# Kernel tuning notes

Hardware: AMD Instinct MI355X
Metric: run time of the kernel (lower is better)

## Reference

```python
import jax, jax.numpy as jnp
import numpy as np

GRID_SIZE = 8
SCALE_SPLINE = 0.1
BATCH, IN_F, OUT_F = 2048, 1024, 1024


def setup_inputs() -> dict:
    key = jax.random.key(0)
    k1, k2, k3 = jax.random.split(key, 3)
    x = jax.random.normal(k1, (BATCH, IN_F), dtype=jnp.float32)
    # kaiming-uniform-ish scale for base linear weight
    bound = 1.0 / np.sqrt(IN_F)
    base_weight = jax.random.uniform(k2, (OUT_F, IN_F), dtype=jnp.float32,
                                     minval=-bound, maxval=bound)
    spline_coeff = 0.1 * jax.random.normal(k3, (OUT_F, IN_F, GRID_SIZE), dtype=jnp.float32)
    # grid buffer: identical linspace(-1,1,G+1) for every (out,in); keep 1-D
    grid = jnp.linspace(-1.0, 1.0, GRID_SIZE + 1, dtype=jnp.float32)
    return {"x": x, "base_weight": base_weight, "spline_coeff": spline_coeff, "grid": grid}


def reference(x, base_weight, spline_coeff, grid):
    # x: (B, I); base_weight: (O, I); spline_coeff: (O, I, G); grid: (G+1,)
    G = spline_coeff.shape[-1]
    base_out = x @ base_weight.T                       # (B, O)

    xc = jnp.clip(x, -1.0, 1.0)                        # (B, I)
    # bucketize: number of grid knots <= xc, minus 1, clamped to valid bin
    mask = xc[..., None] >= grid                       # (B, I, G+1)
    left_idx = jnp.clip(mask.sum(axis=-1) - 1, 0, G - 1)  # (B, I) int

    left_grid = grid[left_idx]                         # (B, I)
    right_grid = grid[left_idx + 1]                    # (B, I)
    denom = right_grid - left_grid
    denom = jnp.where(denom == 0, jnp.ones_like(denom), denom)
    weight = (xc - left_grid) / denom                  # (B, I)

    # coeff gather + weighted sum over in_features, expressed as a dense
    # contraction against a weight-scaled one-hot of the bin index:
    # spline_out[b,o] = sum_i spline_coeff[o,i,idx[b,i]] * weight[b,i]
    onehot_w = jax.nn.one_hot(left_idx, G, dtype=x.dtype) * weight[..., None]  # (B, I, G)
    spline_out = jnp.einsum('big,oig->bo', onehot_w, spline_coeff)             # (B, O)

    return base_out + SCALE_SPLINE * spline_out
```

## Files before the change

kernel.cpp:

```cpp
#include <hip/hip_runtime.h>
#include <stdint.h>

#define BATCH 2048
#define INF 1024
#define OUTF 1024
#define GRID_G 8
#define KTOT 9216

#define BM 256
#define BN 256
#define BK 64
#define SK 8
#define KC (KTOT / SK)
#define NKT (KC / BK)
#define MTT (BATCH / BM)
#define NTT (OUTF / BN)
#define CSLAB ((size_t)BATCH * OUTF)

typedef __attribute__((ext_vector_type(8))) short short8_t;
typedef __attribute__((ext_vector_type(4))) float f32x4_t;
typedef __attribute__((ext_vector_type(8))) unsigned short u16x8_t;

__device__ __forceinline__ unsigned short f2bf(float f) {
  unsigned int u = __float_as_uint(f);
  u += 0x7FFFu + ((u >> 16) & 1u);
  return (unsigned short)(u >> 16);
}

__device__ __forceinline__ void async16(void* lds, const void* g) {
  __builtin_amdgcn_global_load_lds(
      (const __attribute__((address_space(1))) void*)g,
      (__attribute__((address_space(3))) void*)lds, 16, 0, 0);
}

__global__ __launch_bounds__(256) void build_w_kernel(
    const float* __restrict__ bw, const float* __restrict__ coeff,
    unsigned short* __restrict__ wc) {
  int id = blockIdx.x * 256 + threadIdx.x;
  int row = id / (KTOT / 8);
  int k8 = id - row * (KTOT / 8);
  int k = k8 * 8;
  const float* src = (k < INF) ? (bw + (size_t)row * INF + k)
                               : (coeff + (size_t)row * (INF * GRID_G) + (k - INF));
  const float4* s4 = (const float4*)src;
  float4 a = s4[0], b = s4[1];
  u16x8_t v;
  v[0] = f2bf(a.x); v[1] = f2bf(a.y); v[2] = f2bf(a.z); v[3] = f2bf(a.w);
  v[4] = f2bf(b.x); v[5] = f2bf(b.y); v[6] = f2bf(b.z); v[7] = f2bf(b.w);
  *(u16x8_t*)(wc + (size_t)id * 8) = v;
}

__global__ __launch_bounds__(256) void build_a_kernel(
    const float* __restrict__ x, const float* __restrict__ grid,
    unsigned short* __restrict__ ac) {
  __shared__ float sg[GRID_G + 1];
  if (threadIdx.x <= GRID_G) sg[threadIdx.x] = grid[threadIdx.x];
  __syncthreads();
  int id = blockIdx.x * 256 + threadIdx.x;
  int b = id >> 10;
  int i = id & 1023;
  float xv = x[id];
  ac[(size_t)b * KTOT + i] = f2bf(xv);
  float xc = fminf(fmaxf(xv, -1.0f), 1.0f);
  int cnt = 0;
#pragma unroll
  for (int j = 0; j <= GRID_G; ++j) cnt += (xc >= sg[j]) ? 1 : 0;
  int idx = cnt - 1;
  idx = idx < 0 ? 0 : (idx > GRID_G - 1 ? GRID_G - 1 : idx);
  float left = sg[idx], right = sg[idx + 1];
  float denom = right - left;
  denom = (denom == 0.0f) ? 1.0f : denom;
  float w = (xc - left) / denom;
  unsigned short val = f2bf(0.1f * w);
  u16x8_t v;
#pragma unroll
  for (int g = 0; g < GRID_G; ++g) v[g] = (g == idx) ? val : (unsigned short)0;
  *(u16x8_t*)(ac + (size_t)b * KTOT + INF + (size_t)i * 8) = v;
}

__global__ __launch_bounds__(512, 2) void gemm_kernel(
    const unsigned short* __restrict__ A, const unsigned short* __restrict__ W,
    unsigned short* __restrict__ P) {
  __shared__ unsigned short LA[2][2][256 * 32];
  __shared__ unsigned short LB[2][2][256 * 32];

  int bid = blockIdx.x;
  int sk = bid & 7;
  int t0 = bid >> 3;
  int mt = t0 >> 2;
  int nt = t0 & 3;

  int tid = threadIdx.x;
  int wave = tid >> 6;
  int lane = tid & 63;
  int wr = wave >> 2, wc = wave & 3;
  int lr = lane & 15, lk = lane >> 4;
  int rlo = lk * 128 + lr * 8;

  int srow = (tid >> 6) * 16 + (tid & 15);
  int scol = ((tid >> 4) & 3) * 8;
  const unsigned short* gA  = A + (size_t)(mt * BM + srow) * KTOT + sk * KC + scol;
  const unsigned short* gA2 = gA + (size_t)128 * KTOT;
  const unsigned short* gB  = W + (size_t)(nt * BN + srow) * KTOT + sk * KC + scol;
  const unsigned short* gB2 = gB + (size_t)128 * KTOT;

  f32x4_t acc[2][4][4];
#pragma unroll
  for (int ch = 0; ch < 2; ++ch)
#pragma unroll
    for (int mf = 0; mf < 4; ++mf)
#pragma unroll
      for (int nf = 0; nf < 4; ++nf) acc[ch][mf][nf] = f32x4_t{0.f, 0.f, 0.f, 0.f};

#define STAGE_A(nb, ks_, tt) { \
    unsigned short* d_ = &LA[nb][ks_][wave * 512]; \
    async16(d_, gA + (tt) * BK + (ks_) * 32); \
    async16(d_ + 4096, gA2 + (tt) * BK + (ks_) * 32); }
#define STAGE_B(nb, ks_, tt) { \
    unsigned short* d_ = &LB[nb][ks_][wave * 512]; \
    async16(d_, gB + (tt) * BK + (ks_) * 32); \
    async16(d_ + 4096, gB2 + (tt) * BK + (ks_) * 32); }
#define LOAD_BF(ks_) { _Pragma("unroll") for (int nf = 0; nf < 4; ++nf) \
    bfr[nf] = *(const short8_t*)&LB[c][ks_][(wc * 4 + nf) * 512 + rlo]; }
#define LOAD_AF(ks_, ch_) { _Pragma("unroll") for (int mf = 0; mf < 4; ++mf) \
    afr[mf] = *(const short8_t*)&LA[c][ks_][(wr * 8 + (ch_) * 4 + mf) * 512 + rlo]; }
#define DO_MFMA(ch_) { __builtin_amdgcn_s_setprio(1); \
    _Pragma("unroll") for (int mf = 0; mf < 4; ++mf) \
    _Pragma("unroll") for (int nf = 0; nf < 4; ++nf) \
      acc[ch_][mf][nf] = __builtin_amdgcn_mfma_f32_16x16x32_bf16( \
          afr[mf], bfr[nf], acc[ch_][mf][nf], 0, 0, 0); \
    __builtin_amdgcn_s_setprio(0); }
#define GATE(pf_) { if (pf_) asm volatile("s_waitcnt vmcnt(4)" ::: "memory"); \
    else asm volatile("s_waitcnt vmcnt(0)" ::: "memory"); \
    __builtin_amdgcn_s_barrier(); \
    asm volatile("" ::: "memory"); }

  STAGE_A(0, 0, 0) STAGE_B(0, 0, 0) STAGE_A(0, 1, 0) STAGE_B(0, 1, 0)

  for (int t = 0; t < NKT; ++t) {
    int c = t & 1, nb = c ^ 1;
    int tn = t + 1;
    bool pf = tn < NKT;
    short8_t afr[4], bfr[4];

    GATE(pf)
    LOAD_AF(0, 0) LOAD_BF(0)
    if (pf) STAGE_A(nb, 0, tn)
    DO_MFMA(0)
    LOAD_AF(0, 1)
    if (pf) STAGE_B(nb, 0, tn)
    DO_MFMA(1)

    GATE(pf)
    LOAD_AF(1, 0) LOAD_BF(1)
    if (pf) STAGE_A(nb, 1, tn)
    DO_MFMA(0)
    LOAD_AF(1, 1)
    if (pf) STAGE_B(nb, 1, tn)
    DO_MFMA(1)
  }

  unsigned short* slab = P + (size_t)sk * CSLAB;
#pragma unroll
  for (int ch = 0; ch < 2; ++ch)
#pragma unroll
    for (int mf = 0; mf < 4; ++mf)
#pragma unroll
      for (int nf = 0; nf < 4; ++nf) {
        int col = nt * BN + wc * 64 + nf * 16 + lr;
        int rowb = mt * BM + wr * 128 + ch * 64 + mf * 16 + lk * 4;
#pragma unroll
        for (int r = 0; r < 4; ++r)
          slab[(size_t)(rowb + r) * OUTF + col] = f2bf(acc[ch][mf][nf][r]);
      }
}

__global__ __launch_bounds__(256) void reduce_kernel(
    const unsigned short* __restrict__ P, float* __restrict__ out) {
  size_t base = ((size_t)blockIdx.x * 256 + threadIdx.x) * 8;
  float s[8];
#pragma unroll
  for (int j = 0; j < 8; ++j) s[j] = 0.0f;
#pragma unroll
  for (int k = 0; k < SK; ++k) {
    u16x8_t v = *(const u16x8_t*)(P + (size_t)k * CSLAB + base);
#pragma unroll
    for (int j = 0; j < 8; ++j)
      s[j] += __uint_as_float((unsigned int)v[j] << 16);
  }
  float4 lo = {s[0], s[1], s[2], s[3]};
  float4 hi = {s[4], s[5], s[6], s[7]};
  *(float4*)(out + base) = lo;
  *(float4*)(out + base + 4) = hi;
}

extern "C" void kernel_launch(void* const* d_in, const int* in_sizes, int n_in,
                              void* d_out, int out_size, void* d_ws, size_t ws_size,
                              hipStream_t stream) {
  const float* x = (const float*)d_in[0];
  const float* bw = (const float*)d_in[1];
  const float* coeff = (const float*)d_in[2];
  const float* grid = (const float*)d_in[3];
  float* out = (float*)d_out;

  unsigned short* Acat = (unsigned short*)d_ws;
  unsigned short* Wcat = Acat + (size_t)BATCH * KTOT;
  unsigned short* Part = Wcat + (size_t)OUTF * KTOT;

  build_w_kernel<<<OUTF * (KTOT / 8) / 256, 256, 0, stream>>>(bw, coeff, Wcat);
  build_a_kernel<<<BATCH * INF / 256, 256, 0, stream>>>(x, grid, Acat);
  gemm_kernel<<<SK * MTT * NTT, 512, 0, stream>>>(Acat, Wcat, Part);
  reduce_kernel<<<(int)(CSLAB / 8 / 256), 256, 0, stream>>>(Part, out);
}
```

Before: 76.62 us.

## Restructure GEMM main loop into barrier-fenced phases with split LDS buffers

Replaces the indexed double-buffered LDS arrays with eight separately named buffers and unrolls the K loop by two, so buffer selection is static. Each K-half is split into phases. Every phase issues its LDS fragment reads and the next async global-to-LDS stage, then waits on lgkmcnt behind a sched_barrier and runs the MFMA block between two workgroup barriers. The vmcnt waits are moved to the B-staging phases. The aim is to make LDS reads, global prefetch and MFMA issue interleave more predictably across waves. The cost is many more barriers per K tile, which adds synchronisation stalls.

```diff
diff --git a/kernel.cpp b/kernel.cpp
--- a/kernel.cpp
+++ b/kernel.cpp
@@ -81,8 +81,10 @@
 __global__ __launch_bounds__(512, 2) void gemm_kernel(
     const unsigned short* __restrict__ A, const unsigned short* __restrict__ W,
     unsigned short* __restrict__ P) {
-  __shared__ unsigned short LA[2][2][256 * 32];
-  __shared__ unsigned short LB[2][2][256 * 32];
+  __shared__ unsigned short A0K0[256 * 32], A0K1[256 * 32];
+  __shared__ unsigned short A1K0[256 * 32], A1K1[256 * 32];
+  __shared__ unsigned short B0K0[256 * 32], B0K1[256 * 32];
+  __shared__ unsigned short B1K0[256 * 32], B1K1[256 * 32];
 
   int bid = blockIdx.x;
   int sk = bid & 7;
@@ -112,52 +114,60 @@
 #pragma unroll
       for (int nf = 0; nf < 4; ++nf) acc[ch][mf][nf] = f32x4_t{0.f, 0.f, 0.f, 0.f};
 
-#define STAGE_A(nb, ks_, tt) { \
-    unsigned short* d_ = &LA[nb][ks_][wave * 512]; \
-    async16(d_, gA + (tt) * BK + (ks_) * 32); \
-    async16(d_ + 4096, gA2 + (tt) * BK + (ks_) * 32); }
-#define STAGE_B(nb, ks_, tt) { \
-    unsigned short* d_ = &LB[nb][ks_][wave * 512]; \
-    async16(d_, gB + (tt) * BK + (ks_) * 32); \
-    async16(d_ + 4096, gB2 + (tt) * BK + (ks_) * 32); }
-#define LOAD_BF(ks_) { _Pragma("unroll") for (int nf = 0; nf < 4; ++nf) \
-    bfr[nf] = *(const short8_t*)&LB[c][ks_][(wc * 4 + nf) * 512 + rlo]; }
-#define LOAD_AF(ks_, ch_) { _Pragma("unroll") for (int mf = 0; mf < 4; ++mf) \
-    afr[mf] = *(const short8_t*)&LA[c][ks_][(wr * 8 + (ch_) * 4 + mf) * 512 + rlo]; }
-#define DO_MFMA(ch_) { __builtin_amdgcn_s_setprio(1); \
+#define DSR_AF(ARR, CH) { _Pragma("unroll") for (int mf = 0; mf < 4; ++mf) \
+    af[mf] = *(const short8_t*)&ARR[(wr * 8 + (CH) * 4 + mf) * 512 + rlo]; }
+#define DSR_BF(ARR) { _Pragma("unroll") for (int nf = 0; nf < 4; ++nf) \
+    bf[nf] = *(const short8_t*)&ARR[(wc * 4 + nf) * 512 + rlo]; }
+#define STAGE(DARR, CO) { \
+    unsigned short* d_ = &DARR[wave * 512]; \
+    async16(d_, gA_sel + (CO)); \
+    async16(d_ + 4096, gA2_sel + (CO)); }
+#define STAGEA(DARR, CO) { unsigned short* d_ = &DARR[wave * 512]; \
+    async16(d_, gA + (CO)); async16(d_ + 4096, gA2 + (CO)); }
+#define STAGEB(DARR, CO) { unsigned short* d_ = &DARR[wave * 512]; \
+    async16(d_, gB + (CO)); async16(d_ + 4096, gB2 + (CO)); }
+#define BAR() __builtin_amdgcn_s_barrier();
+#define LGKM0() { asm volatile("s_waitcnt lgkmcnt(0)" ::: "memory"); \
+    __builtin_amdgcn_sched_barrier(0); }
+#define MFMA16(CH) { __builtin_amdgcn_s_setprio(1); \
     _Pragma("unroll") for (int mf = 0; mf < 4; ++mf) \
     _Pragma("unroll") for (int nf = 0; nf < 4; ++nf) \
-      acc[ch_][mf][nf] = __builtin_amdgcn_mfma_f32_16x16x32_bf16( \
-          afr[mf], bfr[nf], acc[ch_][mf][nf], 0, 0, 0); \
+      acc[CH][mf][nf] = __builtin_amdgcn_mfma_f32_16x16x32_bf16( \
+          af[mf], bf[nf], acc[CH][mf][nf], 0, 0, 0); \
     __builtin_amdgcn_s_setprio(0); }
-#define GATE(pf_) { if (pf_) asm volatile("s_waitcnt vmcnt(4)" ::: "memory"); \
-    else asm volatile("s_waitcnt vmcnt(0)" ::: "memory"); \
-    __builtin_amdgcn_s_barrier(); \
-    asm volatile("" ::: "memory"); }
-
-  STAGE_A(0, 0, 0) STAGE_B(0, 0, 0) STAGE_A(0, 1, 0) STAGE_B(0, 1, 0)
-
-  for (int t = 0; t < NKT; ++t) {
-    int c = t & 1, nb = c ^ 1;
-    int tn = t + 1;
-    bool pf = tn < NKT;
-    short8_t afr[4], bfr[4];
-
-    GATE(pf)
-    LOAD_AF(0, 0) LOAD_BF(0)
-    if (pf) STAGE_A(nb, 0, tn)
-    DO_MFMA(0)
-    LOAD_AF(0, 1)
-    if (pf) STAGE_B(nb, 0, tn)
-    DO_MFMA(1)
-
-    GATE(pf)
-    LOAD_AF(1, 0) LOAD_BF(1)
-    if (pf) STAGE_A(nb, 1, tn)
-    DO_MFMA(0)
-    LOAD_AF(1, 1)
-    if (pf) STAGE_B(nb, 1, tn)
-    DO_MFMA(1)
+#define VM(pf_) { if (pf_) asm volatile("s_waitcnt vmcnt(4)" ::: "memory"); \
+    else asm volatile("s_waitcnt vmcnt(0)" ::: "memory"); }
+
+#define TILE(CA0, CA1, CB0, CB1, NA0, NA1, NB0, NB1, tt, pf_) { \
+    short8_t af[4], bf[4]; \
+    int ko = ((tt) + 1) * BK; \
+     \
+    DSR_BF(CB0) DSR_AF(CA0, 0) \
+    if (pf_) STAGEA(NA0, ko) \
+    BAR() LGKM0() MFMA16(0) BAR() \
+     \
+    DSR_AF(CA0, 1) \
+    if (pf_) STAGEB(NB0, ko) \
+    VM(pf_) BAR() LGKM0() MFMA16(1) BAR() \
+     \
+    DSR_BF(CB1) DSR_AF(CA1, 0) \
+    if (pf_) STAGEA(NA1, ko + 32) \
+    BAR() LGKM0() MFMA16(0) BAR() \
+     \
+    DSR_AF(CA1, 1) \
+    if (pf_) STAGEB(NB1, ko + 32) \
+    VM(pf_) BAR() LGKM0() MFMA16(1) BAR() \
+}
+
+  STAGEA(A0K0, 0) STAGEB(B0K0, 0) STAGEA(A0K1, 32) STAGEB(B0K1, 32)
+  VM(1)
+  BAR()
+
+  for (int i = 0; i < NKT / 2; ++i) {
+    int te = 2 * i, to = 2 * i + 1;
+    bool pfo = (to + 1) < NKT;
+    TILE(A0K0, A0K1, B0K0, B0K1, A1K0, A1K1, B1K0, B1K1, te, true)
+    TILE(A1K0, A1K1, B1K0, B1K1, A0K0, A0K1, B0K0, B0K1, to, pfo)
   }
 
   unsigned short* slab = P + (size_t)sk * CSLAB;
```

Result: slower. 81.19 us (+6.0%).

## Expand spline one-hot A operand in registers instead of materializing it

Applied to the files above, without the earlier changes.

The 9216-wide concatenated A matrix (bf16 x plus an 8-wide one-hot spline block) is no longer written out. The prep kernel now emits bf16 x and a packed 32-bit (weight, bin index) word per element. The GEMM stages these packed words into LDS and expands them into one-hot MFMA fragments in registers. This removes most of the A-side global write and read traffic. The cost is ALU work per fragment and a hand-unrolled, more intricate pipeline with custom waitcnt schedules.

```diff
diff --git a/kernel.cpp b/kernel.cpp
--- a/kernel.cpp
+++ b/kernel.cpp
@@ -7,14 +7,9 @@
 #define GRID_G 8
 #define KTOT 9216
 
-#define BM 256
-#define BN 256
-#define BK 64
 #define SK 8
-#define KC (KTOT / SK)
-#define NKT (KC / BK)
-#define MTT (BATCH / BM)
-#define NTT (OUTF / BN)
+#define MTT 8
+#define NTT 4
 #define CSLAB ((size_t)BATCH * OUTF)
 
 typedef __attribute__((ext_vector_type(8))) short short8_t;
@@ -31,6 +26,19 @@
   __builtin_amdgcn_global_load_lds(
       (const __attribute__((address_space(1))) void*)g,
       (__attribute__((address_space(3))) void*)lds, 16, 0, 0);
+}
+
+__device__ __forceinline__ short8_t onehot_frag(unsigned int p) {
+  unsigned int wlo = p & 0xFFFFu;
+  unsigned int idx = p >> 16;
+  unsigned int sel = (idx & 1u) ? (wlo << 16) : wlo;
+  unsigned int jt = idx >> 1;
+  union { unsigned int u[4]; short8_t s; } r;
+  r.u[0] = (jt == 0u) ? sel : 0u;
+  r.u[1] = (jt == 1u) ? sel : 0u;
+  r.u[2] = (jt == 2u) ? sel : 0u;
+  r.u[3] = (jt == 3u) ? sel : 0u;
+  return r.s;
 }
 
 __global__ __launch_bounds__(256) void build_w_kernel(
@@ -50,17 +58,15 @@
   *(u16x8_t*)(wc + (size_t)id * 8) = v;
 }
 
-__global__ __launch_bounds__(256) void build_a_kernel(
+__global__ __launch_bounds__(256) void build_apack_kernel(
     const float* __restrict__ x, const float* __restrict__ grid,
-    unsigned short* __restrict__ ac) {
+    unsigned short* __restrict__ xbf, unsigned int* __restrict__ ap) {
   __shared__ float sg[GRID_G + 1];
   if (threadIdx.x <= GRID_G) sg[threadIdx.x] = grid[threadIdx.x];
   __syncthreads();
   int id = blockIdx.x * 256 + threadIdx.x;
-  int b = id >> 10;
-  int i = id & 1023;
   float xv = x[id];
-  ac[(size_t)b * KTOT + i] = f2bf(xv);
+  xbf[id] = f2bf(xv);
   float xc = fminf(fmaxf(xv, -1.0f), 1.0f);
   int cnt = 0;
 #pragma unroll
@@ -71,38 +77,39 @@
   float denom = right - left;
   denom = (denom == 0.0f) ? 1.0f : denom;
   float w = (xc - left) / denom;
-  unsigned short val = f2bf(0.1f * w);
-  u16x8_t v;
-#pragma unroll
-  for (int g = 0; g < GRID_G; ++g) v[g] = (g == idx) ? val : (unsigned short)0;
-  *(u16x8_t*)(ac + (size_t)b * KTOT + INF + (size_t)i * 8) = v;
-}
-
-__global__ __launch_bounds__(512, 2) void gemm_kernel(
-    const unsigned short* __restrict__ A, const unsigned short* __restrict__ W,
-    unsigned short* __restrict__ P) {
+  ap[id] = (unsigned int)f2bf(0.1f * w) | ((unsigned int)idx << 16);
+}
+
+__global__ __launch_bounds__(512, 2) void fused_gemm_kernel(
+    const unsigned short* __restrict__ Xb, const unsigned int* __restrict__ Ap,
+    const unsigned short* __restrict__ Wc, unsigned short* __restrict__ P) {
   __shared__ unsigned short LA[2][2][256 * 32];
   __shared__ unsigned short LB[2][2][256 * 32];
 
   int bid = blockIdx.x;
   int sk = bid & 7;
-  int t0 = bid >> 3;
-  int mt = t0 >> 2;
-  int nt = t0 & 3;
-
-  int tid = threadIdx.x;
-  int wave = tid >> 6;
-  int lane = tid & 63;
+  int t0i = bid >> 3;
+  int mt = t0i >> 2, nt = t0i & 3;
+
+  int tid = threadIdx.x, wave = tid >> 6, lane = tid & 63;
   int wr = wave >> 2, wc = wave & 3;
   int lr = lane & 15, lk = lane >> 4;
   int rlo = lk * 128 + lr * 8;
 
-  int srow = (tid >> 6) * 16 + (tid & 15);
-  int scol = ((tid >> 4) & 3) * 8;
-  const unsigned short* gA  = A + (size_t)(mt * BM + srow) * KTOT + sk * KC + scol;
-  const unsigned short* gA2 = gA + (size_t)128 * KTOT;
-  const unsigned short* gB  = W + (size_t)(nt * BN + srow) * KTOT + sk * KC + scol;
-  const unsigned short* gB2 = gB + (size_t)128 * KTOT;
+  int srow = wave * 16 + (lane & 15);
+  int scol = ((lane >> 4) & 3) * 8;
+  const unsigned short* gXA  = Xb + (size_t)(mt * 256 + srow) * INF + sk * 128 + scol;
+  const unsigned short* gXA2 = gXA + (size_t)128 * INF;
+  const unsigned short* gB   = Wc + (size_t)(nt * 256 + srow) * KTOT + scol;
+  const unsigned short* gB2  = gB + (size_t)128 * KTOT;
+  const unsigned int* gAP = Ap + (size_t)(mt * 256 + wave * 32 + (lane >> 1)) * INF
+                            + sk * 128 + (lane & 1) * 4;
+
+  unsigned int* APK0 = (unsigned int*)&LA[0][0][0];
+  unsigned int* APK1 = (unsigned int*)&LA[1][0][0];
+
+  const int CB = sk * 128;
+  const int CS = 1024 + sk * 1024;
 
   f32x4_t acc[2][4][4];
 #pragma unroll
@@ -112,52 +119,88 @@
 #pragma unroll
       for (int nf = 0; nf < 4; ++nf) acc[ch][mf][nf] = f32x4_t{0.f, 0.f, 0.f, 0.f};
 
-#define STAGE_A(nb, ks_, tt) { \
-    unsigned short* d_ = &LA[nb][ks_][wave * 512]; \
-    async16(d_, gA + (tt) * BK + (ks_) * 32); \
-    async16(d_ + 4096, gA2 + (tt) * BK + (ks_) * 32); }
-#define STAGE_B(nb, ks_, tt) { \
-    unsigned short* d_ = &LB[nb][ks_][wave * 512]; \
-    async16(d_, gB + (tt) * BK + (ks_) * 32); \
-    async16(d_ + 4096, gB2 + (tt) * BK + (ks_) * 32); }
-#define LOAD_BF(ks_) { _Pragma("unroll") for (int nf = 0; nf < 4; ++nf) \
-    bfr[nf] = *(const short8_t*)&LB[c][ks_][(wc * 4 + nf) * 512 + rlo]; }
-#define LOAD_AF(ks_, ch_) { _Pragma("unroll") for (int mf = 0; mf < 4; ++mf) \
-    afr[mf] = *(const short8_t*)&LA[c][ks_][(wr * 8 + (ch_) * 4 + mf) * 512 + rlo]; }
-#define DO_MFMA(ch_) { __builtin_amdgcn_s_setprio(1); \
+#define VMW(N) asm volatile("s_waitcnt vmcnt(" #N ")" ::: "memory")
+#define BARR() { __builtin_amdgcn_s_barrier(); asm volatile("" ::: "memory"); }
+#define STAGE_XA(nb, ks, colofs) { unsigned short* d_ = &LA[nb][ks][wave * 512]; \
+    async16(d_, gXA + (colofs) + (ks) * 32); \
+    async16(d_ + 4096, gXA2 + (colofs) + (ks) * 32); }
+#define STAGE_B(nb, ks, colofs) { unsigned short* d_ = &LB[nb][ks][wave * 512]; \
+    async16(d_, gB + (colofs) + (ks) * 32); \
+    async16(d_ + 4096, gB2 + (colofs) + (ks) * 32); }
+#define STAGE_APK(APKn, tt) { async16((void*)((APKn) + wave * 256), gAP + ((tt) - 2) * 8); }
+#define DSR_A(af_, CC, ks, ch) { _Pragma("unroll") for (int mf = 0; mf < 4; ++mf) \
+    af_[mf] = *(const short8_t*)&LA[CC][ks][(wr * 8 + (ch) * 4 + mf) * 512 + rlo]; }
+#define DSR_B(bf_, CC, ks) { _Pragma("unroll") for (int nf = 0; nf < 4; ++nf) \
+    bf_[nf] = *(const short8_t*)&LB[CC][ks][(wc * 4 + nf) * 512 + rlo]; }
+#define PRD(pr_, APKc, ks, ch) { _Pragma("unroll") for (int mf = 0; mf < 4; ++mf) \
+    pr_[mf] = (APKc)[(wr * 128 + (ch) * 64 + mf * 16 + lr) * 8 + (ks) * 4 + lk]; }
+#define EXPAND(af_, pr_) { _Pragma("unroll") for (int mf = 0; mf < 4; ++mf) \
+    af_[mf] = onehot_frag(pr_[mf]); }
+#define MFMA16(CH, af_, bf_) { __builtin_amdgcn_s_setprio(1); \
     _Pragma("unroll") for (int mf = 0; mf < 4; ++mf) \
     _Pragma("unroll") for (int nf = 0; nf < 4; ++nf) \
-      acc[ch_][mf][nf] = __builtin_amdgcn_mfma_f32_16x16x32_bf16( \
-          afr[mf], bfr[nf], acc[ch_][mf][nf], 0, 0, 0); \
+      acc[CH][mf][nf] = __builtin_amdgcn_mfma_f32_16x16x32_bf16( \
+          af_[mf], bf_[nf], acc[CH][mf][nf], 0, 0, 0); \
     __builtin_amdgcn_s_setprio(0); }
-#define GATE(pf_) { if (pf_) asm volatile("s_waitcnt vmcnt(4)" ::: "memory"); \
-    else asm volatile("s_waitcnt vmcnt(0)" ::: "memory"); \
-    __builtin_amdgcn_s_barrier(); \
-    asm volatile("" ::: "memory"); }
-
-  STAGE_A(0, 0, 0) STAGE_B(0, 0, 0) STAGE_A(0, 1, 0) STAGE_B(0, 1, 0)
-
-  for (int t = 0; t < NKT; ++t) {
-    int c = t & 1, nb = c ^ 1;
-    int tn = t + 1;
-    bool pf = tn < NKT;
-    short8_t afr[4], bfr[4];
-
-    GATE(pf)
-    LOAD_AF(0, 0) LOAD_BF(0)
-    if (pf) STAGE_A(nb, 0, tn)
-    DO_MFMA(0)
-    LOAD_AF(0, 1)
-    if (pf) STAGE_B(nb, 0, tn)
-    DO_MFMA(1)
-
-    GATE(pf)
-    LOAD_AF(1, 0) LOAD_BF(1)
-    if (pf) STAGE_A(nb, 1, tn)
-    DO_MFMA(0)
-    LOAD_AF(1, 1)
-    if (pf) STAGE_B(nb, 1, tn)
-    DO_MFMA(1)
+
+  STAGE_XA(0, 0, 0) STAGE_B(0, 0, CB) STAGE_XA(0, 1, 0) STAGE_B(0, 1, CB)
+
+  {
+    short8_t af[4], bf[4];
+    VMW(4); BARR();
+    DSR_A(af, 0, 0, 0) DSR_B(bf, 0, 0)
+    STAGE_XA(1, 0, 64)
+    MFMA16(0, af, bf)
+    DSR_A(af, 0, 0, 1)
+    STAGE_B(1, 0, CB + 64)
+    MFMA16(1, af, bf)
+    VMW(4); BARR();
+    DSR_A(af, 0, 1, 0) DSR_B(bf, 0, 1)
+    STAGE_XA(1, 1, 64)
+    MFMA16(0, af, bf)
+    DSR_A(af, 0, 1, 1)
+    STAGE_B(1, 1, CB + 64)
+    MFMA16(1, af, bf)
+  }
+  {
+    short8_t af[4], bf[4];
+    VMW(4); BARR();
+    DSR_A(af, 1, 0, 0) DSR_B(bf, 1, 0)
+    STAGE_APK(APK0, 2)
+    MFMA16(0, af, bf)
+    DSR_A(af, 1, 0, 1)
+    STAGE_B(0, 0, CS)
+    MFMA16(1, af, bf)
+    VMW(3); BARR();
+    DSR_A(af, 1, 1, 0) DSR_B(bf, 1, 1)
+    STAGE_B(0, 1, CS)
+    MFMA16(0, af, bf)
+    DSR_A(af, 1, 1, 1)
+    MFMA16(1, af, bf)
+  }
+  for (int t = 2; t < 18; ++t) {
+    int c = t & 1;
+    unsigned int* APKc = c ? APK1 : APK0;
+    unsigned int* APKn = c ? APK0 : APK1;
+    int nb = c ^ 1;
+    bool pf = t < 17;
+    int cs = CS + (t - 1) * 64;
+    short8_t af[4], bf[4];
+    unsigned int pr[4];
+    VMW(2); BARR();
+    PRD(pr, APKc, 0, 0) DSR_B(bf, c, 0)
+    if (pf) STAGE_APK(APKn, t + 1)
+    EXPAND(af, pr) MFMA16(0, af, bf)
+    PRD(pr, APKc, 0, 1)
+    if (pf) STAGE_B(nb, 0, cs)
+    EXPAND(af, pr) MFMA16(1, af, bf)
+    if (pf) { VMW(3); } else { VMW(0); }
+    BARR();
+    PRD(pr, APKc, 1, 0) DSR_B(bf, c, 1)
+    if (pf) STAGE_B(nb, 1, cs)
+    EXPAND(af, pr) MFMA16(0, af, bf)
+    PRD(pr, APKc, 1, 1)
+    EXPAND(af, pr) MFMA16(1, af, bf)
   }
 
   unsigned short* slab = P + (size_t)sk * CSLAB;
@@ -167,8 +210,8 @@
     for (int mf = 0; mf < 4; ++mf)
 #pragma unroll
       for (int nf = 0; nf < 4; ++nf) {
-        int col = nt * BN + wc * 64 + nf * 16 + lr;
-        int rowb = mt * BM + wr * 128 + ch * 64 + mf * 16 + lk * 4;
+        int col = nt * 256 + wc * 64 + nf * 16 + lr;
+        int rowb = mt * 256 + wr * 128 + ch * 64 + mf * 16 + lk * 4;
 #pragma unroll
         for (int r = 0; r < 4; ++r)
           slab[(size_t)(rowb + r) * OUTF + col] = f2bf(acc[ch][mf][nf][r]);
@@ -203,12 +246,13 @@
   const float* grid = (const float*)d_in[3];
   float* out = (float*)d_out;
 
-  unsigned short* Acat = (unsigned short*)d_ws;
-  unsigned short* Wcat = Acat + (size_t)BATCH * KTOT;
-  unsigned short* Part = Wcat + (size_t)OUTF * KTOT;
+  unsigned short* Wcat = (unsigned short*)d_ws;
+  unsigned short* Xbf  = Wcat + (size_t)OUTF * KTOT;
+  unsigned int*   Apack = (unsigned int*)(Xbf + (size_t)BATCH * INF);
+  unsigned short* Part = (unsigned short*)(Apack + (size_t)BATCH * INF);
 
   build_w_kernel<<<OUTF * (KTOT / 8) / 256, 256, 0, stream>>>(bw, coeff, Wcat);
-  build_a_kernel<<<BATCH * INF / 256, 256, 0, stream>>>(x, grid, Acat);
-  gemm_kernel<<<SK * MTT * NTT, 512, 0, stream>>>(Acat, Wcat, Part);
+  build_apack_kernel<<<BATCH * INF / 256, 256, 0, stream>>>(x, grid, Xbf, Apack);
+  fused_gemm_kernel<<<SK * MTT * NTT, 512, 0, stream>>>(Xbf, Apack, Wcat, Part);
   reduce_kernel<<<(int)(CSLAB / 8 / 256), 256, 0, stream>>>(Part, out);
 }
```

New measurement: 71.33 us. -6.9%, faster.
